# Optimization experiments

Hardware: AMD Instinct MI355X
Metric: run time of the kernel (lower is better)

## Reference

```python
import jax, jax.numpy as jnp
import numpy as np

E = 1024   # embed_dim
H = 16     # num_heads
DH = E // H
FF = 4096  # intermediate_size
EPS = 1e-5


def layernorm(x, g, b):
    mu = jnp.mean(x, axis=-1, keepdims=True)
    var = jnp.var(x, axis=-1, keepdims=True)
    return (x - mu) * jax.lax.rsqrt(var + EPS) * g + b


def setup_inputs() -> dict:
    key = jax.random.key(0)
    ks = jax.random.split(key, 16)
    s = 0.02
    return {
        "x": jax.random.normal(ks[0], (2, 2048, E), dtype=jnp.float32),
        "ln1_g": jnp.ones((E,), jnp.float32),
        "ln1_b": jnp.zeros((E,), jnp.float32),
        "ln2_g": jnp.ones((E,), jnp.float32),
        "ln2_b": jnp.zeros((E,), jnp.float32),
        # per-head Q/K/V projections stacked: [H, E, DH]
        "wq": jax.random.normal(ks[1], (H, E, DH), jnp.float32) * s,
        "bq": jnp.zeros((H, DH), jnp.float32),
        "wk": jax.random.normal(ks[2], (H, E, DH), jnp.float32) * s,
        "bk": jnp.zeros((H, DH), jnp.float32),
        "wv": jax.random.normal(ks[3], (H, E, DH), jnp.float32) * s,
        "bv": jnp.zeros((H, DH), jnp.float32),
        "wo": jax.random.normal(ks[4], (E, E), jnp.float32) * s,
        "bo": jnp.zeros((E,), jnp.float32),
        "w1": jax.random.normal(ks[5], (E, FF), jnp.float32) * s,
        "b1": jnp.zeros((FF,), jnp.float32),
        "w2": jax.random.normal(ks[6], (FF, E), jnp.float32) * s,
        "b2": jnp.zeros((E,), jnp.float32),
    }


def reference(x, ln1_g, ln1_b, ln2_g, ln2_b, wq, bq, wk, bk, wv, bv,
              wo, bo, w1, b1, w2, b2):
    # --- multi-head attention (pre-LN) ---
    h = layernorm(x, ln1_g, ln1_b)                       # [B,S,E]
    q = jnp.einsum('bse,hed->bhsd', h, wq) + bq[:, None, :]
    k = jnp.einsum('bse,hed->bhsd', h, wk) + bk[:, None, :]
    v = jnp.einsum('bse,hed->bhsd', h, wv) + bv[:, None, :]
    scores = jnp.einsum('bhsd,bhtd->bhst', q, k) / jnp.sqrt(
        jnp.asarray(DH, x.dtype))                        # [B,H,S,S]
    w = jax.nn.softmax(scores, axis=-1)
    attn = jnp.einsum('bhst,bhtd->bhsd', w, v)           # [B,H,S,DH]
    B, _, S, _ = attn.shape
    concat = attn.transpose(0, 2, 1, 3).reshape(B, S, E)  # head concat order
    x = x + concat @ wo + bo
    # --- feed-forward (pre-LN), exact GELU, dropout_p=0 ---
    h2 = layernorm(x, ln2_g, ln2_b)
    ff = jax.nn.gelu(h2 @ w1 + b1, approximate=False) @ w2 + b2
    return x + ff
```

## Files before the change

kernel.cpp:

```cpp
#include <hip/hip_runtime.h>
#include <hip/hip_bf16.h>
#include <math.h>

typedef __attribute__((ext_vector_type(8))) short short8;
typedef __attribute__((ext_vector_type(4))) float f32x4;
typedef __attribute__((ext_vector_type(16))) float f32x16;
typedef __attribute__((ext_vector_type(4))) unsigned u32x4;

#define MFMA_BF16(a, b, c) __builtin_amdgcn_mfma_f32_16x16x32_bf16(a, b, c, 0, 0, 0)
#define MFMA32_BF16(a, b, c) __builtin_amdgcn_mfma_f32_32x32x16_bf16(a, b, c, 0, 0, 0)

#define GLD_LDS16(g, l)                                              \
  __builtin_amdgcn_global_load_lds(                                  \
      (const __attribute__((address_space(1))) void*)(g),            \
      (__attribute__((address_space(3))) void*)(l), 16, 0, 0)

template <int N>
__device__ __forceinline__ void waitcnt_vm() {
  if constexpr (N == 0) asm volatile("s_waitcnt vmcnt(0)" ::: "memory");
  else if constexpr (N == 4) asm volatile("s_waitcnt vmcnt(4)" ::: "memory");
  else if constexpr (N == 6) asm volatile("s_waitcnt vmcnt(6)" ::: "memory");
  else if constexpr (N == 8) asm volatile("s_waitcnt vmcnt(8)" ::: "memory");
}

__device__ __forceinline__ unsigned cvt_pk_bf16(float lo, float hi) {
  unsigned r;
  asm("v_cvt_pk_bf16_f32 %0, %1, %2" : "=v"(r) : "v"(lo), "v"(hi));
  return r;
}
#define PSWAP(a, b) asm volatile("v_permlane32_swap_b32 %0, %1" : "+v"(a), "+v"(b))

__device__ __forceinline__ unsigned short f2bf(float f) {
  union { float f; unsigned u; } v; v.f = f;
  unsigned r = v.u + 0x7FFFu + ((v.u >> 16) & 1u);
  return (unsigned short)(r >> 16);
}
__device__ __forceinline__ float bf2f(unsigned short u) {
  union { unsigned u; float f; } v; v.u = ((unsigned)u) << 16;
  return v.f;
}

__global__ __launch_bounds__(256) void transpose_cast(
    const float* __restrict__ in, unsigned short* __restrict__ out,
    int R, int C, size_t in_bs, size_t out_bs) {
  __shared__ float t[32][33];
  const float* inp = in + blockIdx.z * in_bs;
  unsigned short* outp = out + blockIdx.z * out_bs;
  const int c0 = blockIdx.x * 32, r0 = blockIdx.y * 32;
  const int tx = threadIdx.x, ty = threadIdx.y;
#pragma unroll
  for (int i = 0; i < 32; i += 8)
    t[ty + i][tx] = inp[(size_t)(r0 + ty + i) * C + c0 + tx];
  __syncthreads();
#pragma unroll
  for (int i = 0; i < 32; i += 8)
    outp[(size_t)(c0 + ty + i) * R + r0 + tx] = f2bf(t[tx][ty + i]);
}

__global__ void concat_bias(const float* __restrict__ bq, const float* __restrict__ bk,
                            const float* __restrict__ bv, float* __restrict__ bcat) {
  int i = blockIdx.x * 256 + threadIdx.x;
  if (i < 1024) bcat[i] = bq[i];
  else if (i < 2048) bcat[i] = bk[i - 1024];
  else if (i < 3072) bcat[i] = bv[i - 2048];
}

__global__ __launch_bounds__(512) void vtrans(
    const unsigned short* __restrict__ qkv, unsigned short* __restrict__ vt) {
  __shared__ unsigned short t[64][65];
  const int bh = blockIdx.y;
  const int s0 = blockIdx.x * 64;
  const int tx = threadIdx.x;
  const int ty = threadIdx.y;
  const unsigned short* in =
      qkv + (size_t)(bh >> 4) * 2048 * 3072 + 2048 + (bh & 15) * 64;
#pragma unroll
  for (int i = 0; i < 8; ++i)
    t[ty * 8 + i][tx] = in[(size_t)(s0 + ty * 8 + i) * 3072 + tx];
  __syncthreads();
  unsigned short* o = vt + (size_t)bh * 64 * 2048 + s0;
#pragma unroll
  for (int i = 0; i < 8; ++i)
    o[(size_t)(ty * 8 + i) * 2048 + tx] = t[tx][ty * 8 + i];
}

__global__ __launch_bounds__(256) void ln_kernel(
    const float* __restrict__ x, const float* __restrict__ g,
    const float* __restrict__ bb, unsigned short* __restrict__ out) {
  const int row = blockIdx.x, tid = threadIdx.x;
  const float4 v = ((const float4*)(x + (size_t)row * 1024))[tid];
  float s = v.x + v.y + v.z + v.w;
  float ss = v.x * v.x + v.y * v.y + v.z * v.z + v.w * v.w;
#pragma unroll
  for (int k = 1; k < 64; k <<= 1) {
    s += __shfl_xor(s, k, 64);
    ss += __shfl_xor(ss, k, 64);
  }
  __shared__ float red[8];
  const int wid = tid >> 6;
  if ((tid & 63) == 0) { red[wid] = s; red[wid + 4] = ss; }
  __syncthreads();
  s = red[0] + red[1] + red[2] + red[3];
  ss = red[4] + red[5] + red[6] + red[7];
  const float mu = s * (1.0f / 1024.0f);
  const float var = ss * (1.0f / 1024.0f) - mu * mu;
  const float rs = rsqrtf(var + 1e-5f);
  const float4 gv = ((const float4*)g)[tid];
  const float4 bv = ((const float4*)bb)[tid];
  ushort4 o;
  o.x = f2bf((v.x - mu) * rs * gv.x + bv.x);
  o.y = f2bf((v.y - mu) * rs * gv.y + bv.y);
  o.z = f2bf((v.z - mu) * rs * gv.z + bv.z);
  o.w = f2bf((v.w - mu) * rs * gv.w + bv.w);
  ((ushort4*)(out + (size_t)row * 1024))[tid] = o;
}

template <int EPI, int BN>
__global__ __launch_bounds__(256, (BN == 128) ? 2 : 3) void gemm_bt(
    const unsigned short* __restrict__ A, const unsigned short* __restrict__ Bt,
    const float* __restrict__ bias, const float* __restrict__ res,
    void* __restrict__ Cout, int M, int N, int K) {
  constexpr int NFR = BN / 32;
  constexpr int BISS = BN / 32;
  constexpr int ISS = 4 + BISS;
  __shared__ unsigned short As[2][128 * 64];
  __shared__ unsigned short Bs[2][BN * 64];
  const int tid = threadIdx.x;
  const int wid = tid >> 6, lane = tid & 63;
  const int li = lane & 15, gi = lane >> 4;
  const int bm = blockIdx.y, bn = blockIdx.x;
  const int wr = (wid >> 1) << 6;
  const int wc = (wid & 1) * (BN / 2);

  f32x4 acc[4][NFR];
#pragma unroll
  for (int m = 0; m < 4; ++m)
#pragma unroll
    for (int n = 0; n < NFR; ++n) acc[m][n] = (f32x4)0.0f;

  const size_t Ksz = (size_t)K;
  const int srow = tid >> 3;
  const int segG = (tid & 7) ^ (srow & 7);
  const unsigned short* Ab = A + (size_t)(bm * 128 + srow) * Ksz + segG * 8;
  const unsigned short* Bb = Bt + (size_t)(bn * BN + srow) * Ksz + segG * 8;

  auto stage = [&](int buf, int kt) {
#pragma unroll
    for (int c = 0; c < 4; ++c)
      GLD_LDS16(Ab + (size_t)(c * 32) * Ksz + kt, &As[buf][c * 2048 + wid * 512]);
#pragma unroll
    for (int c = 0; c < BISS; ++c)
      GLD_LDS16(Bb + (size_t)(c * 32) * Ksz + kt, &Bs[buf][c * 2048 + wid * 512]);
  };

  auto compute = [&](int ib) {
    const unsigned short* As_ = As[ib];
    const unsigned short* Bs_ = Bs[ib];
    short8 af[4][2], bf[NFR][2];
#pragma unroll
    for (int m = 0; m < 4; ++m)
#pragma unroll
      for (int kk = 0; kk < 2; ++kk) {
        const int row = wr + m * 16 + li;
        af[m][kk] = *(const short8*)(As_ + row * 64 + ((kk * 4 + gi) ^ (row & 7)) * 8);
      }
#pragma unroll
    for (int n = 0; n < NFR; ++n)
#pragma unroll
      for (int kk = 0; kk < 2; ++kk) {
        const int row = wc + n * 16 + li;
        bf[n][kk] = *(const short8*)(Bs_ + row * 64 + ((kk * 4 + gi) ^ (row & 7)) * 8);
      }
    __builtin_amdgcn_s_setprio(1);
#pragma unroll
    for (int m = 0; m < 4; ++m)
#pragma unroll
      for (int n = 0; n < NFR; ++n) {
        acc[m][n] = MFMA_BF16(af[m][0], bf[n][0], acc[m][n]);
        acc[m][n] = MFMA_BF16(af[m][1], bf[n][1], acc[m][n]);
      }
    __builtin_amdgcn_s_setprio(0);
  };

  const int KT = K >> 6;
  stage(0, 0);
  for (int i = 0; i < KT - 1; ++i) {
    stage((i + 1) & 1, (i + 1) << 6);
    waitcnt_vm<ISS>();
    __builtin_amdgcn_s_barrier();
    __builtin_amdgcn_sched_barrier(0);
    compute(i & 1);
    __builtin_amdgcn_s_barrier();
  }
  waitcnt_vm<0>();
  __builtin_amdgcn_s_barrier();
  __builtin_amdgcn_sched_barrier(0);
  compute((KT - 1) & 1);

  const int row_base = bm * 128 + wr + gi * 4;
  const int col_base = bn * BN + wc + li;
#pragma unroll
  for (int m = 0; m < 4; ++m) {
#pragma unroll
    for (int n = 0; n < NFR; ++n) {
      const int col = col_base + n * 16;
      const float bi = bias[col];
#pragma unroll
      for (int r = 0; r < 4; ++r) {
        const int row = row_base + m * 16 + r;
        float v = acc[m][n][r] + bi;
        if (EPI == 2) v = 0.5f * v * (1.0f + erff(v * 0.70710678118654752f));
        const size_t idx = (size_t)row * N + col;
        if (EPI == 1) ((float*)Cout)[idx] = v + res[idx];
        else ((unsigned short*)Cout)[idx] = f2bf(v);
      }
    }
  }
}

__global__ __launch_bounds__(256, 4) void attn_kernel(
    const unsigned short* __restrict__ qkv, const unsigned short* __restrict__ vt,
    unsigned short* __restrict__ op0, unsigned short* __restrict__ op1,
    float* __restrict__ lpart) {
  __shared__ unsigned short Kl[2][4096];
  __shared__ unsigned short Vl[2][4096];
  const int tid = threadIdx.x;
  const int wid = tid >> 6, lane = tid & 63;
  const int l31 = lane & 31, hiq = lane >> 5;
  const int kvh = blockIdx.z & 1, b = blockIdx.z >> 1, h = blockIdx.y;
  const int q0 = blockIdx.x * 128 + wid * 32;
  const int LD = 3072;
  const size_t base = (size_t)b * 2048 * LD;
  const size_t kvoff = (size_t)kvh * 1024 * LD;

  short8 qb[4];
  {
    const unsigned short* qp = qkv + base + (size_t)(q0 + l31) * LD + h * 64 + hiq * 8;
#pragma unroll
    for (int ds = 0; ds < 4; ++ds) qb[ds] = *(const short8*)(qp + ds * 16);
  }

  f32x16 o0 = (f32x16)0.0f, o1 = (f32x16)0.0f;
  float la = 0.0f, lb = 0.0f;

  const int rw = lane >> 3;
  const int sgG = (lane & 7) ^ rw;
  const unsigned short* kdma = qkv + base + kvoff + 1024 + h * 64 + sgG * 8 +
                               (size_t)(wid * 16 + rw) * LD;
  const unsigned short* vdma = vt + (size_t)(b * 16 + h) * 64 * 2048 +
                               (size_t)(wid * 16 + rw) * 2048 + kvh * 1024 + sgG * 8;

  auto kstage = [&](int buf, int t) {
    GLD_LDS16(kdma + (size_t)t * 64 * LD, &Kl[buf][wid * 1024]);
    GLD_LDS16(kdma + (size_t)(t * 64 + 8) * LD, &Kl[buf][wid * 1024 + 512]);
  };
  auto vstage = [&](int buf, int t) {
    GLD_LDS16(vdma + t * 64, &Vl[buf][wid * 1024]);
    GLD_LDS16(vdma + 8 * 2048 + t * 64, &Vl[buf][wid * 1024 + 512]);
  };

  auto compute = [&](int ib) {
    const unsigned short* kl = Kl[ib];
    const unsigned short* vl = Vl[ib];
    short8 kf[2][4];
#pragma unroll
    for (int kvb = 0; kvb < 2; ++kvb)
#pragma unroll
      for (int ds = 0; ds < 4; ++ds)
        kf[kvb][ds] = *(const short8*)(
            kl + (kvb * 32 + l31) * 64 + (((2 * ds + hiq) ^ (l31 & 7)) * 8));

    f32x16 sA = (f32x16)0.0f, sB = (f32x16)0.0f;
    __builtin_amdgcn_s_setprio(1);
#pragma unroll
    for (int ds = 0; ds < 4; ++ds) {
      sA = MFMA32_BF16(kf[0][ds], qb[ds], sA);
      sB = MFMA32_BF16(kf[1][ds], qb[ds], sB);
    }
    __builtin_amdgcn_s_setprio(0);

#pragma unroll
    for (int kvb = 0; kvb < 2; ++kvb) {
      const f32x16 s = kvb ? sB : sA;
      unsigned P[8];
#pragma unroll
      for (int i = 0; i < 8; ++i) {
        const float pe = __expf(s[2 * i] * 0.125f);
        const float po = __expf(s[2 * i + 1] * 0.125f);
        la += pe; lb += po;
        P[i] = cvt_pk_bf16(pe, po);
      }
      PSWAP(P[0], P[2]); PSWAP(P[1], P[3]);
      PSWAP(P[4], P[6]); PSWAP(P[5], P[7]);
      const short8 pa0 = __builtin_bit_cast(short8, (u32x4){P[0], P[1], P[2], P[3]});
      const short8 pa1 = __builtin_bit_cast(short8, (u32x4){P[4], P[5], P[6], P[7]});
      const int sg0 = 4 * kvb + hiq, sg1 = 4 * kvb + 2 + hiq;
      const short8 v00 = *(const short8*)(vl + l31 * 64 + ((sg0 ^ (l31 & 7)) * 8));
      const short8 v01 = *(const short8*)(vl + l31 * 64 + ((sg1 ^ (l31 & 7)) * 8));
      const short8 v10 = *(const short8*)(vl + (32 + l31) * 64 + ((sg0 ^ (l31 & 7)) * 8));
      const short8 v11 = *(const short8*)(vl + (32 + l31) * 64 + ((sg1 ^ (l31 & 7)) * 8));
      __builtin_amdgcn_s_setprio(1);
      o0 = MFMA32_BF16(pa0, v00, o0);
      o0 = MFMA32_BF16(pa1, v01, o0);
      o1 = MFMA32_BF16(pa0, v10, o1);
      o1 = MFMA32_BF16(pa1, v11, o1);
      __builtin_amdgcn_s_setprio(0);
    }
  };

  kstage(0, 0);
  vstage(0, 0);
  for (int t = 0; t < 15; ++t) {
    kstage((t + 1) & 1, t + 1);
    vstage((t + 1) & 1, t + 1);
    waitcnt_vm<4>();
    __builtin_amdgcn_s_barrier();
    __builtin_amdgcn_sched_barrier(0);
    compute(t & 1);
    __builtin_amdgcn_s_barrier();
  }
  waitcnt_vm<0>();
  __builtin_amdgcn_s_barrier();
  __builtin_amdgcn_sched_barrier(0);
  compute(15 & 1);

  const float lsum = la + lb;
  const float lt = lsum + __shfl_xor(lsum, 32, 64);
  if (hiq == 0)
    lpart[(size_t)kvh * 65536 + ((size_t)(b * 2048 + q0 + l31) * 16) + h] = lt;

  unsigned short* op = kvh ? op1 : op0;
#pragma unroll
  for (int r = 0; r < 16; ++r) {
    const int crow = (r & 3) + 8 * (r >> 2) + 4 * hiq;
    const size_t rowb = (size_t)(b * 2048 + q0 + crow) * 1024 + h * 64 + l31;
    op[rowb]      = f2bf(o0[r]);
    op[rowb + 32] = f2bf(o1[r]);
  }
}

__global__ __launch_bounds__(256) void attn_combine(
    const unsigned short* __restrict__ op0, unsigned short* __restrict__ op1io,
    const float* __restrict__ lpart) {
  const size_t i8 = (size_t)blockIdx.x * 256 + threadIdx.x;
  const size_t g = (i8 * 8) >> 6;
  const float inv = 1.0f / (lpart[g] + lpart[g + 65536]);
  const short8 a = *(const short8*)(op0 + i8 * 8);
  const short8 c = *(const short8*)(op1io + i8 * 8);
  short8 o;
#pragma unroll
  for (int j = 0; j < 8; ++j)
    o[j] = (short)f2bf((bf2f((unsigned short)a[j]) + bf2f((unsigned short)c[j])) * inv);
  *(short8*)(op1io + i8 * 8) = o;
}

extern "C" void kernel_launch(void* const* d_in, const int* in_sizes, int n_in,
                              void* d_out, int out_size, void* d_ws, size_t ws_size,
                              hipStream_t stream) {
  const float* x     = (const float*)d_in[0];
  const float* ln1_g = (const float*)d_in[1];
  const float* ln1_b = (const float*)d_in[2];
  const float* ln2_g = (const float*)d_in[3];
  const float* ln2_b = (const float*)d_in[4];
  const float* wq    = (const float*)d_in[5];
  const float* bq    = (const float*)d_in[6];
  const float* wk    = (const float*)d_in[7];
  const float* bk    = (const float*)d_in[8];
  const float* wv    = (const float*)d_in[9];
  const float* bv    = (const float*)d_in[10];
  const float* wo    = (const float*)d_in[11];
  const float* bo    = (const float*)d_in[12];
  const float* w1    = (const float*)d_in[13];
  const float* b1    = (const float*)d_in[14];
  const float* w2    = (const float*)d_in[15];
  const float* b2    = (const float*)d_in[16];
  float* out = (float*)d_out;

  char* p = (char*)d_ws;
  unsigned short* ws_h     = (unsigned short*)p; p += 4096ull * 1024 * 2;
  unsigned short* ws_qkv   = (unsigned short*)p; p += 4096ull * 3072 * 2;
  unsigned short* ws_attn  = (unsigned short*)p; p += 4096ull * 1024 * 2;
  unsigned short* ws_wqkvT = (unsigned short*)p; p += 3072ull * 1024 * 2;
  unsigned short* ws_woT   = (unsigned short*)p; p += 1024ull * 1024 * 2;
  unsigned short* ws_w1T   = (unsigned short*)p; p += 4096ull * 1024 * 2;
  unsigned short* ws_w2T   = (unsigned short*)p; p += 1024ull * 4096 * 2;
  float*          ws_bqkv  = (float*)p;          p += 3072 * 4;
  float*          ws_l     = (float*)p;          p += 2ull * 65536 * 4;
  unsigned short* ws_ff = ws_qkv;
  unsigned short* ws_vt = ws_w1T;

  const dim3 tb(32, 8);
  transpose_cast<<<dim3(2, 32, 16), tb, 0, stream>>>(
      wq, ws_wqkvT, 1024, 64, (size_t)(1024 * 64), (size_t)(64 * 1024));
  transpose_cast<<<dim3(2, 32, 16), tb, 0, stream>>>(
      wk, ws_wqkvT + 1024ull * 1024, 1024, 64, (size_t)(1024 * 64), (size_t)(64 * 1024));
  transpose_cast<<<dim3(2, 32, 16), tb, 0, stream>>>(
      wv, ws_wqkvT + 2048ull * 1024, 1024, 64, (size_t)(1024 * 64), (size_t)(64 * 1024));
  transpose_cast<<<dim3(32, 32, 1), tb, 0, stream>>>(wo, ws_woT, 1024, 1024, 0, 0);
  concat_bias<<<12, 256, 0, stream>>>(bq, bk, bv, ws_bqkv);

  ln_kernel<<<4096, 256, 0, stream>>>(x, ln1_g, ln1_b, ws_h);
  gemm_bt<0, 128><<<dim3(24, 32), 256, 0, stream>>>(ws_h, ws_wqkvT, ws_bqkv, nullptr,
                                                    ws_qkv, 4096, 3072, 1024);
  vtrans<<<dim3(32, 32), dim3(64, 8), 0, stream>>>(ws_qkv, ws_vt);
  attn_kernel<<<dim3(16, 16, 4), 256, 0, stream>>>(ws_qkv, ws_vt, ws_h, ws_attn, ws_l);
  attn_combine<<<2048, 256, 0, stream>>>(ws_h, ws_attn, ws_l);
  transpose_cast<<<dim3(128, 32, 1), tb, 0, stream>>>(w1, ws_w1T, 1024, 4096, 0, 0);
  transpose_cast<<<dim3(32, 128, 1), tb, 0, stream>>>(w2, ws_w2T, 4096, 1024, 0, 0);
  gemm_bt<1, 64><<<dim3(16, 32), 256, 0, stream>>>(ws_attn, ws_woT, bo, x,
                                                   out, 4096, 1024, 1024);
  ln_kernel<<<4096, 256, 0, stream>>>(out, ln2_g, ln2_b, ws_h);
  gemm_bt<2, 128><<<dim3(32, 32), 256, 0, stream>>>(ws_h, ws_w1T, b1, nullptr,
                                                    ws_ff, 4096, 4096, 1024);
  gemm_bt<1, 64><<<dim3(16, 32), 256, 0, stream>>>(ws_ff, ws_w2T, b2, out,
                                                   out, 4096, 1024, 4096);
}
```

Baseline: 264.3 us.

## Add 256x256-tile 8-wave GEMM with interleaved prefetch for QKV and FF1

Adds a new gemm256 kernel that uses 512 threads and 256x256 output tiles held in 128KB of dynamic LDS with double buffering. Global-to-LDS loads are staggered between quarter-tile MFMA groups, with barriers and setprio between them. It replaces the 128x128 gemm_bt for the QKV projection and the FF1+GELU GEMM. This raises data reuse per tile but leaves fewer blocks (192 and 256) to spread across CUs and adds heavy register pressure.

```diff
diff --git a/kernel.cpp b/kernel.cpp
--- a/kernel.cpp
+++ b/kernel.cpp
@@ -9,6 +9,7 @@
 
 #define MFMA_BF16(a, b, c) __builtin_amdgcn_mfma_f32_16x16x32_bf16(a, b, c, 0, 0, 0)
 #define MFMA32_BF16(a, b, c) __builtin_amdgcn_mfma_f32_32x32x16_bf16(a, b, c, 0, 0, 0)
+#define BAR() __builtin_amdgcn_s_barrier()
 
 #define GLD_LDS16(g, l)                                              \
   __builtin_amdgcn_global_load_lds(                                  \
@@ -18,6 +19,7 @@
 template <int N>
 __device__ __forceinline__ void waitcnt_vm() {
   if constexpr (N == 0) asm volatile("s_waitcnt vmcnt(0)" ::: "memory");
+  else if constexpr (N == 2) asm volatile("s_waitcnt vmcnt(2)" ::: "memory");
   else if constexpr (N == 4) asm volatile("s_waitcnt vmcnt(4)" ::: "memory");
   else if constexpr (N == 6) asm volatile("s_waitcnt vmcnt(6)" ::: "memory");
   else if constexpr (N == 8) asm volatile("s_waitcnt vmcnt(8)" ::: "memory");
@@ -113,6 +115,130 @@
   o.z = f2bf((v.z - mu) * rs * gv.z + bv.z);
   o.w = f2bf((v.w - mu) * rs * gv.w + bv.w);
   ((ushort4*)(out + (size_t)row * 1024))[tid] = o;
+}
+
+template <int QM, int QN>
+__device__ __forceinline__ void mfq(f32x4 (&acc)[8][4], short8 (&af)[4][2],
+                                    short8 (&bf)[2][2]) {
+  __builtin_amdgcn_s_setprio(1);
+#pragma unroll
+  for (int i = 0; i < 4; ++i)
+#pragma unroll
+    for (int nf = 0; nf < 2; ++nf) {
+      acc[QM * 4 + i][QN * 2 + nf] =
+          MFMA_BF16(af[i][0], bf[nf][0], acc[QM * 4 + i][QN * 2 + nf]);
+      acc[QM * 4 + i][QN * 2 + nf] =
+          MFMA_BF16(af[i][1], bf[nf][1], acc[QM * 4 + i][QN * 2 + nf]);
+    }
+  __builtin_amdgcn_s_setprio(0);
+}
+
+template <int EPI>
+__global__ __launch_bounds__(512, 2) void gemm256(
+    const unsigned short* __restrict__ A, const unsigned short* __restrict__ Bt,
+    const float* __restrict__ bias, void* __restrict__ Cout,
+    int M, int N, int K) {
+  extern __shared__ unsigned short L[];
+  const int tid = threadIdx.x;
+  const int wv = tid >> 6, lane = tid & 63;
+  const int li = lane & 15, gi = lane >> 4;
+  const int wm = wv >> 2, wn = wv & 3;
+  const int bm = blockIdx.y, bn = blockIdx.x;
+  const size_t Ksz = (size_t)K;
+  const int KT = K >> 6;
+
+  auto lds = [&](int buf, int op, int half) -> unsigned short* {
+    return L + (size_t)(((buf * 2 + op) * 2 + half)) * 8192;
+  };
+
+  const int sr8 = tid >> 3;
+  const int segG = (tid & 7) ^ (sr8 & 7);
+  const unsigned short* Ag = A + (size_t)(bm * 256 + sr8) * Ksz + segG * 8;
+  const unsigned short* Bg = Bt + (size_t)(bn * 256 + sr8) * Ksz + segG * 8;
+  const int wbase = wv * 512;
+
+  auto stg = [&](int buf, int op, int half, int tile) {
+    const unsigned short* g =
+        (op ? Bg : Ag) + (size_t)(half * 128) * Ksz + (tile % KT) * 64;
+    unsigned short* d = lds(buf, op, half);
+    GLD_LDS16(g, d + wbase);
+    GLD_LDS16(g + (size_t)64 * Ksz, d + 4096 + wbase);
+  };
+
+  f32x4 acc[8][4];
+#pragma unroll
+  for (int m = 0; m < 8; ++m)
+#pragma unroll
+    for (int n = 0; n < 4; ++n) acc[m][n] = (f32x4)0.0f;
+
+  short8 af[4][2], b0[2][2], b1[2][2];
+  auto ldA = [&](int buf, int qm) {
+    const unsigned short* p = lds(buf, 0, wm);
+#pragma unroll
+    for (int i = 0; i < 4; ++i) {
+      const int r = qm * 64 + i * 16 + li;
+#pragma unroll
+      for (int kk = 0; kk < 2; ++kk)
+        af[i][kk] = *(const short8*)(p + r * 64 + (((kk * 4 + gi) ^ (r & 7)) * 8));
+    }
+  };
+  auto ldB = [&](short8 (&bf)[2][2], int buf, int qn) {
+    const unsigned short* p = lds(buf, 1, wn >> 1);
+#pragma unroll
+    for (int nf = 0; nf < 2; ++nf) {
+      const int r = (wn & 1) * 64 + qn * 32 + nf * 16 + li;
+#pragma unroll
+      for (int kk = 0; kk < 2; ++kk)
+        bf[nf][kk] = *(const short8*)(p + r * 64 + (((kk * 4 + gi) ^ (r & 7)) * 8));
+    }
+  };
+
+  stg(0, 0, 0, 0); stg(0, 0, 1, 0); stg(0, 1, 0, 0); stg(0, 1, 1, 0);
+  stg(1, 0, 0, 1);
+
+  for (int j = 0; j < KT / 2; ++j) {
+    const int t1 = 2 * j + 1, t2 = 2 * j + 2, t3 = 2 * j + 3;
+    waitcnt_vm<2>(); BAR();
+    ldA(0, 0); ldB(b0, 0, 0);
+    stg(1, 0, 1, t1); stg(1, 1, 0, t1);
+    BAR(); mfq<0, 0>(acc, af, b0); BAR();
+    ldB(b1, 0, 1);
+    stg(1, 1, 1, t1);
+    BAR(); mfq<0, 1>(acc, af, b1); BAR();
+    ldA(0, 1);
+    stg(0, 0, 0, t2);
+    BAR(); mfq<1, 0>(acc, af, b0); BAR();
+    mfq<1, 1>(acc, af, b1); BAR();
+    waitcnt_vm<2>(); BAR();
+    ldA(1, 0); ldB(b0, 1, 0);
+    stg(0, 0, 1, t2); stg(0, 1, 0, t2);
+    BAR(); mfq<0, 0>(acc, af, b0); BAR();
+    ldB(b1, 1, 1);
+    stg(0, 1, 1, t2);
+    BAR(); mfq<0, 1>(acc, af, b1); BAR();
+    ldA(1, 1);
+    stg(1, 0, 0, t3);
+    BAR(); mfq<1, 0>(acc, af, b0); BAR();
+    mfq<1, 1>(acc, af, b1); BAR();
+  }
+
+  const int row0 = bm * 256 + wm * 128 + gi * 4;
+  const int col0 = bn * 256 + wn * 64 + li;
+#pragma unroll
+  for (int mf = 0; mf < 8; ++mf) {
+#pragma unroll
+    for (int nf = 0; nf < 4; ++nf) {
+      const int col = col0 + nf * 16;
+      const float bi = bias[col];
+#pragma unroll
+      for (int r = 0; r < 4; ++r) {
+        const int row = row0 + mf * 16 + r;
+        float v = acc[mf][nf][r] + bi;
+        if (EPI == 2) v = 0.5f * v * (1.0f + erff(v * 0.70710678118654752f));
+        ((unsigned short*)Cout)[(size_t)row * N + col] = f2bf(v);
+      }
+    }
+  }
 }
 
 template <int EPI, int BN>
@@ -376,6 +502,11 @@
   const float* b2    = (const float*)d_in[16];
   float* out = (float*)d_out;
 
+  hipFuncSetAttribute((const void*)gemm256<0>,
+                      hipFuncAttributeMaxDynamicSharedMemorySize, 131072);
+  hipFuncSetAttribute((const void*)gemm256<2>,
+                      hipFuncAttributeMaxDynamicSharedMemorySize, 131072);
+
   char* p = (char*)d_ws;
   unsigned short* ws_h     = (unsigned short*)p; p += 4096ull * 1024 * 2;
   unsigned short* ws_qkv   = (unsigned short*)p; p += 4096ull * 3072 * 2;
@@ -400,7 +531,7 @@
   concat_bias<<<12, 256, 0, stream>>>(bq, bk, bv, ws_bqkv);
 
   ln_kernel<<<4096, 256, 0, stream>>>(x, ln1_g, ln1_b, ws_h);
-  gemm_bt<0, 128><<<dim3(24, 32), 256, 0, stream>>>(ws_h, ws_wqkvT, ws_bqkv, nullptr,
+  gemm256<0><<<dim3(12, 16), 512, 131072, stream>>>(ws_h, ws_wqkvT, ws_bqkv,
                                                     ws_qkv, 4096, 3072, 1024);
   vtrans<<<dim3(32, 32), dim3(64, 8), 0, stream>>>(ws_qkv, ws_vt);
   attn_kernel<<<dim3(16, 16, 4), 256, 0, stream>>>(ws_qkv, ws_vt, ws_h, ws_attn, ws_l);
@@ -410,7 +541,7 @@
   gemm_bt<1, 64><<<dim3(16, 32), 256, 0, stream>>>(ws_attn, ws_woT, bo, x,
                                                    out, 4096, 1024, 1024);
   ln_kernel<<<4096, 256, 0, stream>>>(out, ln2_g, ln2_b, ws_h);
-  gemm_bt<2, 128><<<dim3(32, 32), 256, 0, stream>>>(ws_h, ws_w1T, b1, nullptr,
+  gemm256<2><<<dim3(16, 16), 512, 131072, stream>>>(ws_h, ws_w1T, b1,
                                                     ws_ff, 4096, 4096, 1024);
   gemm_bt<1, 64><<<dim3(16, 32), 256, 0, stream>>>(ws_ff, ws_w2T, b2, out,
                                                    out, 4096, 1024, 4096);
```

New measurement: 252.6 us. 4.4% less time.
